# Kernel tuning notes

Measured on AMD Instinct MI355X. Metric: run time of the kernel, lower is better.

## Reference

```python
import jax, jax.numpy as jnp
import numpy as np

N = 4096      # number of stocks (token axis)
D = 512       # d_model
H = 8         # nhead
DE = 64       # d_emb
DH = D // H   # head_dim = 64
TEMP = float(np.sqrt(DH))
EPS = 1e-5


def _ln(x, g, b):
    mu = jnp.mean(x, axis=-1, keepdims=True)
    var = jnp.var(x, axis=-1, keepdims=True)
    return (x - mu) * jax.lax.rsqrt(var + EPS) * g + b


def setup_inputs() -> dict:
    key = jax.random.key(0)
    ks = jax.random.split(key, 8)
    init = lambda k, shape, fan: (jax.random.normal(k, shape, jnp.float32) / np.sqrt(fan).astype(np.float32))
    return {
        "x": jax.random.normal(ks[0], (N, D), jnp.float32),
        "industry_emb": jax.random.normal(ks[1], (N, DE), jnp.float32),
        # projection weights stored as [in, out] so y = x @ W
        "Wq": init(ks[2], (D + DE, D), D + DE),
        "Wk": init(ks[3], (D + DE, D), D + DE),
        "Wv": init(ks[4], (D, D), D),
        "g1": jnp.ones((D,), jnp.float32), "b1": jnp.zeros((D,), jnp.float32),
        "g2": jnp.ones((DE,), jnp.float32), "b2": jnp.zeros((DE,), jnp.float32),
        "g3": jnp.ones((D,), jnp.float32), "b3": jnp.zeros((D,), jnp.float32),
        "W_ffn1": init(ks[5], (D, D), D), "b_ffn1": jnp.zeros((D,), jnp.float32),
        "W_ffn2": init(ks[6], (D, D), D), "b_ffn2": jnp.zeros((D,), jnp.float32),
    }


def reference(x, industry_emb, Wq, Wk, Wv, g1, b1, g2, b2, g3, b3,
              W_ffn1, b_ffn1, W_ffn2, b_ffn2):
    xn = _ln(x, g1, b1)                       # [N, D]
    en = _ln(industry_emb, g2, b2)            # [N, DE]
    qk_in = jnp.concatenate([xn, en], axis=-1)  # [N, D+DE]
    q = (qk_in @ Wq).reshape(N, H, DH)
    k = (qk_in @ Wk).reshape(N, H, DH)
    v = (xn @ Wv).reshape(N, H, DH)
    # batched multi-head attention (equivalent to the per-head torch loop)
    scores = jnp.einsum('nhd,mhd->hnm', q, k) / TEMP   # [H, N, N]
    attn = jax.nn.softmax(scores, axis=-1)
    att = jnp.einsum('hnm,mhd->nhd', attn, v).reshape(N, D)
    xt = xn + att
    h = _ln(xt, g3, b3)
    ffn = jax.nn.relu(h @ W_ffn1 + b_ffn1) @ W_ffn2 + b_ffn2
    return xt + ffn
```

## Files before the change

kernel.cpp:

```cpp
#include <hip/hip_runtime.h>

#define NTOK 4096
#define DMODEL 512
#define DEMB 64
#define DCAT 576
#define NHEAD 8
#define DHEAD 64
#define QSCALE 0.18033688011112042f

typedef float f32x4 __attribute__((ext_vector_type(4)));
typedef float f32x16 __attribute__((ext_vector_type(16)));
typedef short s16x8 __attribute__((ext_vector_type(8)));
typedef unsigned short u16;
typedef u16 u16x4 __attribute__((ext_vector_type(4)));
typedef u16 u16x8 __attribute__((ext_vector_type(8)));
typedef unsigned int u32;

__device__ __forceinline__ u16 f2bf(float f) {
  union { float f; unsigned u; } v; v.f = f;
  unsigned r = v.u + 0x7fffu + ((v.u >> 16) & 1u);
  return (u16)(r >> 16);
}

__device__ __forceinline__ float bf2f(u16 u) {
  union { unsigned u; float f; } v; v.u = ((unsigned)u) << 16;
  return v.f;
}

__device__ __forceinline__ u32 cvtpk_bf16(float lo, float hi) {
  u32 r;
  asm("v_cvt_pk_bf16_f32 %0, %1, %2" : "=v"(r) : "v"(lo), "v"(hi));
  return r;
}

__device__ __forceinline__ void gload16(const void* g, void* lds) {
  __builtin_amdgcn_global_load_lds((const __attribute__((address_space(1))) u32*)g,
                                   (__attribute__((address_space(3))) u32*)lds, 16, 0, 0);
}

__global__ void wtrans_kernel(const float* __restrict__ Wq, const float* __restrict__ Wk,
                              const float* __restrict__ Wv, const float* __restrict__ Wf1,
                              const float* __restrict__ Wf2,
                              u16* __restrict__ Tqkv, u16* __restrict__ Tf1, u16* __restrict__ Tf2) {
  __shared__ float tile[64][65];
  int w = blockIdx.z;
  const float* src; u16* dst; int Ksrc, Kdst;
  if (w == 0)      { src = Wq;  dst = Tqkv;              Ksrc = 576; Kdst = 576; }
  else if (w == 1) { src = Wk;  dst = Tqkv + 512 * 576;  Ksrc = 576; Kdst = 576; }
  else if (w == 2) { src = Wv;  dst = Tqkv + 1024 * 576; Ksrc = 512; Kdst = 576; }
  else if (w == 3) { src = Wf1; dst = Tf1;               Ksrc = 512; Kdst = 512; }
  else             { src = Wf2; dst = Tf2;               Ksrc = 512; Kdst = 512; }
  int kb = blockIdx.x * 64;
  if (kb >= Kdst) return;
  int nb = blockIdx.y * 64;
  int tid = threadIdx.x;
  #pragma unroll
  for (int i = 0; i < 16; ++i) {
    int idx = tid + i * 256;
    int r = idx >> 6, c = idx & 63;
    tile[r][c] = (kb + r < Ksrc) ? src[(size_t)(kb + r) * DMODEL + nb + c] : 0.0f;
  }
  __syncthreads();
  #pragma unroll
  for (int i = 0; i < 16; ++i) {
    int idx = tid + i * 256;
    int r = idx >> 6, c = idx & 63;
    dst[(size_t)(nb + r) * Kdst + kb + c] = f2bf(tile[c][r]);
  }
}

__global__ void lnx_kernel(const float* __restrict__ x, const float* __restrict__ g,
                           const float* __restrict__ b, float* __restrict__ xt,
                           u16* __restrict__ qkin) {
  int row = blockIdx.x * 4 + (threadIdx.x >> 6);
  int lane = threadIdx.x & 63;
  const float* xr = x + (size_t)row * DMODEL + lane * 8;
  float v[8];
  float4 a0 = *(const float4*)xr;
  float4 a1 = *(const float4*)(xr + 4);
  v[0]=a0.x; v[1]=a0.y; v[2]=a0.z; v[3]=a0.w; v[4]=a1.x; v[5]=a1.y; v[6]=a1.z; v[7]=a1.w;
  float s = 0.f, ss = 0.f;
  #pragma unroll
  for (int j = 0; j < 8; ++j) { s += v[j]; ss += v[j]*v[j]; }
  #pragma unroll
  for (int off = 32; off > 0; off >>= 1) { s += __shfl_xor(s, off); ss += __shfl_xor(ss, off); }
  float mu = s * (1.0f / DMODEL);
  float var = ss * (1.0f / DMODEL) - mu * mu;
  float rs = rsqrtf(var + 1e-5f);
  float4 g0 = *(const float4*)(g + lane * 8);
  float4 g1v = *(const float4*)(g + lane * 8 + 4);
  float4 b0 = *(const float4*)(b + lane * 8);
  float4 b1v = *(const float4*)(b + lane * 8 + 4);
  float gg[8] = {g0.x,g0.y,g0.z,g0.w,g1v.x,g1v.y,g1v.z,g1v.w};
  float bb[8] = {b0.x,b0.y,b0.z,b0.w,b1v.x,b1v.y,b1v.z,b1v.w};
  float o[8]; u16x8 ob;
  #pragma unroll
  for (int j = 0; j < 8; ++j) { o[j] = (v[j]-mu)*rs*gg[j] + bb[j]; ob[j] = f2bf(o[j]); }
  float* xo = xt + (size_t)row * DMODEL + lane * 8;
  *(float4*)xo = make_float4(o[0],o[1],o[2],o[3]);
  *(float4*)(xo + 4) = make_float4(o[4],o[5],o[6],o[7]);
  *(u16x8*)(qkin + (size_t)row * DCAT + lane * 8) = ob;
}

__global__ void lne_kernel(const float* __restrict__ e, const float* __restrict__ g,
                           const float* __restrict__ b, u16* __restrict__ qkin) {
  int row = blockIdx.x * 4 + (threadIdx.x >> 6);
  int lane = threadIdx.x & 63;
  float v = e[(size_t)row * DEMB + lane];
  float s = v, ss = v * v;
  #pragma unroll
  for (int off = 32; off > 0; off >>= 1) { s += __shfl_xor(s, off); ss += __shfl_xor(ss, off); }
  float mu = s * (1.0f / DEMB);
  float var = ss * (1.0f / DEMB) - mu * mu;
  float rs = rsqrtf(var + 1e-5f);
  float o = (v - mu) * rs * g[lane] + b[lane];
  qkin[(size_t)row * DCAT + DMODEL + lane] = f2bf(o);
}

__global__ void ln3_kernel(float* __restrict__ xt, const float* __restrict__ g,
                           const float* __restrict__ b, u16* __restrict__ hb,
                           const u16* __restrict__ obuf, const float* __restrict__ lbuf) {
  int row = blockIdx.x * 4 + (threadIdx.x >> 6);
  int lane = threadIdx.x & 63;
  int h = lane >> 3;
  int dh0 = (lane & 7) * 8;
  float* xr = xt + (size_t)row * DMODEL + lane * 8;
  float v[8];
  float4 a0 = *(const float4*)xr;
  float4 a1 = *(const float4*)(xr + 4);
  v[0]=a0.x; v[1]=a0.y; v[2]=a0.z; v[3]=a0.w; v[4]=a1.x; v[5]=a1.y; v[6]=a1.z; v[7]=a1.w;
  float osum[8] = {};
  float lsum = 0.f;
  #pragma unroll
  for (int s = 0; s < 4; ++s) {
    size_t hb_idx = (size_t)(s * 8 + h) * NTOK + row;
    u16x8 ov = *(const u16x8*)(obuf + hb_idx * 64 + dh0);
    lsum += lbuf[hb_idx];
    #pragma unroll
    for (int j = 0; j < 8; ++j) osum[j] += bf2f(ov[j]);
  }
  float rcpl = 1.0f / lsum;
  #pragma unroll
  for (int j = 0; j < 8; ++j) v[j] += osum[j] * rcpl;
  *(float4*)xr = make_float4(v[0],v[1],v[2],v[3]);
  *(float4*)(xr + 4) = make_float4(v[4],v[5],v[6],v[7]);
  float s = 0.f, ss = 0.f;
  #pragma unroll
  for (int j = 0; j < 8; ++j) { s += v[j]; ss += v[j]*v[j]; }
  #pragma unroll
  for (int off = 32; off > 0; off >>= 1) { s += __shfl_xor(s, off); ss += __shfl_xor(ss, off); }
  float mu = s * (1.0f / DMODEL);
  float var = ss * (1.0f / DMODEL) - mu * mu;
  float rs = rsqrtf(var + 1e-5f);
  float4 g0 = *(const float4*)(g + lane * 8);
  float4 g1v = *(const float4*)(g + lane * 8 + 4);
  float4 b0 = *(const float4*)(b + lane * 8);
  float4 b1v = *(const float4*)(b + lane * 8 + 4);
  float gg[8] = {g0.x,g0.y,g0.z,g0.w,g1v.x,g1v.y,g1v.z,g1v.w};
  float bb[8] = {b0.x,b0.y,b0.z,b0.w,b1v.x,b1v.y,b1v.z,b1v.w};
  u16x8 ob;
  #pragma unroll
  for (int j = 0; j < 8; ++j) ob[j] = f2bf((v[j]-mu)*rs*gg[j] + bb[j]);
  *(u16x8*)(hb + (size_t)row * DMODEL + lane * 8) = ob;
}

__global__ __launch_bounds__(256) void gemm_qkv_kernel(
    const u16* __restrict__ A, const u16* __restrict__ Bt, u16* __restrict__ outb) {
  __shared__ __align__(16) u16 smem[12288];
  u16* Al = smem;
  u16* Bl = smem + 8192;
  int tid = threadIdx.x, lane = tid & 63, wid = tid >> 6;
  int li = lane & 15, g4 = lane >> 4;
  int n0 = blockIdx.x * 64, m0 = blockIdx.y * 128;
  int wr = (wid >> 1) * 64, wc = (wid & 1) * 32;
  f32x4 acc[4][2] = {};
  for (int k0 = 0; k0 < DCAT; k0 += 64) {
    #pragma unroll
    for (int i = 0; i < 4; ++i) {
      int idx = i * 256 + tid;
      int row = idx >> 3, cb = (idx & 7) * 8;
      gload16(A + (size_t)(m0 + row) * DCAT + k0 + cb, (char*)Al + idx * 16);
    }
    #pragma unroll
    for (int i = 0; i < 2; ++i) {
      int idx = i * 256 + tid;
      int row = idx >> 3, cb = (idx & 7) * 8;
      gload16(Bt + (size_t)(n0 + row) * DCAT + k0 + cb, (char*)Bl + idx * 16);
    }
    __syncthreads();
    #pragma unroll
    for (int kk = 0; kk < 2; ++kk) {
      s16x8 af[4], bfv[2];
      #pragma unroll
      for (int mi = 0; mi < 4; ++mi)
        af[mi] = *(const s16x8*)&Al[(wr + mi * 16 + li) * 64 + kk * 32 + g4 * 8];
      #pragma unroll
      for (int ni = 0; ni < 2; ++ni)
        bfv[ni] = *(const s16x8*)&Bl[(wc + ni * 16 + li) * 64 + kk * 32 + g4 * 8];
      #pragma unroll
      for (int mi = 0; mi < 4; ++mi)
        #pragma unroll
        for (int ni = 0; ni < 2; ++ni)
          acc[mi][ni] = __builtin_amdgcn_mfma_f32_16x16x32_bf16(af[mi], bfv[ni], acc[mi][ni], 0, 0, 0);
    }
    __syncthreads();
  }
  if (n0 < 1024) {
    float scale = (n0 < 512) ? QSCALE : 1.0f;
    int nb = (n0 < 512) ? n0 : n0 - 512;
    u16* dst = outb + ((n0 < 512) ? 0 : (size_t)NTOK * DMODEL);
    #pragma unroll
    for (int mi = 0; mi < 4; ++mi)
      #pragma unroll
      for (int ni = 0; ni < 2; ++ni) {
        int col = nb + wc + ni * 16 + li;
        int h = col >> 6, dh = col & 63;
        #pragma unroll
        for (int r = 0; r < 4; ++r) {
          int row = m0 + wr + mi * 16 + g4 * 4 + r;
          dst[((size_t)h * NTOK + row) * DHEAD + dh] = f2bf(acc[mi][ni][r] * scale);
        }
      }
  } else {
    u16* vT = outb + (size_t)2 * NTOK * DMODEL;
    u16* tp = smem;
    __syncthreads();
    #pragma unroll
    for (int mi = 0; mi < 4; ++mi)
      #pragma unroll
      for (int ni = 0; ni < 2; ++ni) {
        int cl = wc + ni * 16 + li;
        int r0 = wr + mi * 16 + g4 * 4;
        int r0p = (r0 & ~12) | ((r0 & 4) << 1) | ((r0 & 8) >> 1);
        u16x4 pk;
        pk[0] = f2bf(acc[mi][ni][0]); pk[1] = f2bf(acc[mi][ni][1]);
        pk[2] = f2bf(acc[mi][ni][2]); pk[3] = f2bf(acc[mi][ni][3]);
        *(u16x4*)&tp[cl * 136 + r0p] = pk;
      }
    __syncthreads();
    for (int c = tid; c < 1024; c += 256) {
      int cl = c >> 4, seg = c & 15;
      u16x8 v = *(const u16x8*)&tp[cl * 136 + seg * 8];
      *(u16x8*)&vT[(size_t)(n0 - 1024 + cl) * NTOK + m0 + seg * 8] = v;
    }
  }
}

template<int MODE>
__global__ __launch_bounds__(256) void gemm_kernel(
    const u16* __restrict__ A, int lda, const u16* __restrict__ Bt, int K,
    u16* __restrict__ outb, float* __restrict__ outf,
    const float* __restrict__ bias, const float* __restrict__ xt) {
  __shared__ __align__(16) u16 smem[8192];
  u16* Al = smem;
  u16* Bl = smem + 4096;
  int tid = threadIdx.x, lane = tid & 63, wid = tid >> 6;
  int li = lane & 15, g4 = lane >> 4;
  int n0 = blockIdx.x * 64, m0 = blockIdx.y * 64;
  int wr = (wid >> 1) * 32, wc = (wid & 1) * 32;
  f32x4 acc[2][2] = {};
  for (int k0 = 0; k0 < K; k0 += 64) {
    #pragma unroll
    for (int i = 0; i < 2; ++i) {
      int idx = i * 256 + tid;
      int row = idx >> 3, cb = (idx & 7) * 8;
      gload16(A + (size_t)(m0 + row) * lda + k0 + cb, (char*)Al + idx * 16);
    }
    #pragma unroll
    for (int i = 0; i < 2; ++i) {
      int idx = i * 256 + tid;
      int row = idx >> 3, cb = (idx & 7) * 8;
      gload16(Bt + (size_t)(n0 + row) * K + k0 + cb, (char*)Bl + idx * 16);
    }
    __syncthreads();
    #pragma unroll
    for (int kk = 0; kk < 2; ++kk) {
      s16x8 af[2], bfv[2];
      #pragma unroll
      for (int mi = 0; mi < 2; ++mi)
        af[mi] = *(const s16x8*)&Al[(wr + mi * 16 + li) * 64 + kk * 32 + g4 * 8];
      #pragma unroll
      for (int ni = 0; ni < 2; ++ni)
        bfv[ni] = *(const s16x8*)&Bl[(wc + ni * 16 + li) * 64 + kk * 32 + g4 * 8];
      #pragma unroll
      for (int mi = 0; mi < 2; ++mi)
        #pragma unroll
        for (int ni = 0; ni < 2; ++ni)
          acc[mi][ni] = __builtin_amdgcn_mfma_f32_16x16x32_bf16(af[mi], bfv[ni], acc[mi][ni], 0, 0, 0);
    }
    __syncthreads();
  }
  #pragma unroll
  for (int mi = 0; mi < 2; ++mi)
    #pragma unroll
    for (int ni = 0; ni < 2; ++ni) {
      int col = n0 + wc + ni * 16 + li;
      float bv = bias[col];
      #pragma unroll
      for (int r = 0; r < 4; ++r) {
        int row = m0 + wr + mi * 16 + g4 * 4 + r;
        float v = acc[mi][ni][r] + bv;
        if (MODE == 3) {
          v = fmaxf(v, 0.0f);
          outb[(size_t)row * DMODEL + col] = f2bf(v);
        } else {
          outf[(size_t)row * DMODEL + col] = v + xt[(size_t)row * DMODEL + col];
        }
      }
    }
}

__global__ __launch_bounds__(512, 1) void attn_kernel(
    const u16* __restrict__ qh, const u16* __restrict__ kh,
    const u16* __restrict__ vT, u16* __restrict__ obuf, float* __restrict__ lbuf) {
  __shared__ __align__(16) u16 kbufT[2][4096];
  __shared__ __align__(16) u16 vbufT[2][4096];
  int tid = threadIdx.x, lane = tid & 63, w = tid >> 6;
  int lq = lane & 31, h5 = lane >> 5;
  int h = blockIdx.x & 7, ks = (blockIdx.x >> 3) & 3, qt = blockIdx.x >> 5;
  int q0w = qt * 256 + w * 32;
  int ko0 = ks * 1024;
  const u16* qb = qh + ((size_t)h * NTOK + q0w + lq) * DHEAD;
  s16x8 qf[4];
  #pragma unroll
  for (int kc = 0; kc < 4; ++kc)
    qf[kc] = *(const s16x8*)(qb + kc * 16 + h5 * 8);
  f32x16 o[2] = {};
  float lsum = 0.f;
  const char* kh_b = (const char*)(kh + (size_t)h * NTOK * DHEAD);
  const char* v_b = (const char*)(vT + (size_t)h * DHEAD * NTOK);

  auto stage = [&](int c, int ko) {
    int lo6 = tid & 63, r6 = tid >> 6;
    gload16(kh_b + (size_t)(ko + lo6) * 128 + r6 * 16, (char*)&kbufT[c][0] + tid * 16);
    gload16(v_b + (size_t)lo6 * (NTOK * 2) + (size_t)(ko + r6 * 8) * 2,
            (char*)&vbufT[c][0] + tid * 16);
  };

  stage(0, ko0);
  asm volatile("s_waitcnt vmcnt(0)" ::: "memory");
  __builtin_amdgcn_sched_barrier(0);
  __syncthreads();

  for (int t = 0; t < 16; ++t) {
    int cur = t & 1;
    if (t < 15) stage(cur ^ 1, ko0 + (t + 1) * 64);
    const u16* Kl = &kbufT[cur][0];
    const u16* Vl = &vbufT[cur][0];
    #pragma unroll
    for (int kb2 = 0; kb2 < 2; ++kb2) {
      f32x16 st = {};
      #pragma unroll
      for (int kc = 0; kc < 4; ++kc) {
        s16x8 kf = *(const s16x8*)(Kl + ((kc * 2 + h5) * 64 + kb2 * 32 + lq) * 8);
        st = __builtin_amdgcn_mfma_f32_32x32x16_bf16(kf, qf[kc], st, 0, 0, 0);
      }
      float p[16];
      #pragma unroll
      for (int r = 0; r < 16; ++r) { p[r] = __builtin_amdgcn_exp2f(st[r]); lsum += p[r]; }
      #pragma unroll
      for (int cl = 0; cl < 2; ++cl) {
        int b = cl * 8;
        union { u32 wv[4]; s16x8 hv; } pu;
        pu.wv[0] = cvtpk_bf16(p[b + 0], p[b + 1]);
        pu.wv[1] = cvtpk_bf16(p[b + 2], p[b + 3]);
        pu.wv[2] = cvtpk_bf16(p[b + 4], p[b + 5]);
        pu.wv[3] = cvtpk_bf16(p[b + 6], p[b + 7]);
        int kcg = kb2 * 2 + cl;
        #pragma unroll
        for (int dhalf = 0; dhalf < 2; ++dhalf) {
          s16x8 bv = *(const s16x8*)(Vl + ((kcg * 2 + h5) * 64 + dhalf * 32 + lq) * 8);
          o[dhalf] = __builtin_amdgcn_mfma_f32_32x32x16_bf16(pu.hv, bv, o[dhalf], 0, 0, 0);
        }
      }
    }
    if (t < 15) {
      asm volatile("s_waitcnt vmcnt(0)" ::: "memory");
      __builtin_amdgcn_sched_barrier(0);
      __syncthreads();
    }
  }

  lsum += __shfl_xor(lsum, 32);
  size_t slice = (size_t)(ks * 8 + h) * NTOK;
  if (h5 == 0) lbuf[slice + q0w + lq] = lsum;
  u16* ob = obuf + (slice + q0w) * 64;
  #pragma unroll
  for (int dhalf = 0; dhalf < 2; ++dhalf)
    #pragma unroll
    for (int r = 0; r < 16; ++r) {
      int crow = (r & 3) + 8 * (r >> 2) + 4 * h5;
      ob[(size_t)crow * 64 + dhalf * 32 + lq] = f2bf(o[dhalf][r]);
    }
}

extern "C" void kernel_launch(void* const* d_in, const int* in_sizes, int n_in,
                              void* d_out, int out_size, void* d_ws, size_t ws_size,
                              hipStream_t stream) {
  const float* x   = (const float*)d_in[0];
  const float* emb = (const float*)d_in[1];
  const float* Wq  = (const float*)d_in[2];
  const float* Wk  = (const float*)d_in[3];
  const float* Wv  = (const float*)d_in[4];
  const float* g1  = (const float*)d_in[5];
  const float* b1  = (const float*)d_in[6];
  const float* g2  = (const float*)d_in[7];
  const float* b2  = (const float*)d_in[8];
  const float* g3  = (const float*)d_in[9];
  const float* b3  = (const float*)d_in[10];
  const float* Wf1 = (const float*)d_in[11];
  const float* bf1 = (const float*)d_in[12];
  const float* Wf2 = (const float*)d_in[13];
  const float* bf2 = (const float*)d_in[14];
  float* out = (float*)d_out;

  char* ws = (char*)d_ws;
  size_t off = 0;
  auto alloc = [&](size_t bytes) { void* p = ws + off; off += (bytes + 255) & ~255ull; return p; };
  float* xt = (float*)alloc((size_t)NTOK * DMODEL * 4);
  u16* qkin = (u16*)alloc((size_t)NTOK * DCAT * 2);
  u16* hb   = (u16*)alloc((size_t)NTOK * DMODEL * 2);
  u16* r1   = (u16*)alloc((size_t)NTOK * DMODEL * 2);
  u16* qkvh = (u16*)alloc((size_t)3 * NTOK * DMODEL * 2);
  u16* Tqkv = (u16*)alloc((size_t)1536 * DCAT * 2);
  u16* Tf1  = (u16*)alloc((size_t)DMODEL * DMODEL * 2);
  u16* Tf2  = (u16*)alloc((size_t)DMODEL * DMODEL * 2);
  u16* obuf = (u16*)alloc((size_t)4 * NHEAD * NTOK * DHEAD * 2);
  float* lbuf = (float*)alloc((size_t)4 * NHEAD * NTOK * 4);
  u16* qhd = qkvh;
  u16* khd = qkvh + (size_t)NTOK * DMODEL;
  u16* vTd = qkvh + (size_t)2 * NTOK * DMODEL;

  wtrans_kernel<<<dim3(9, 8, 5), 256, 0, stream>>>(Wq, Wk, Wv, Wf1, Wf2, Tqkv, Tf1, Tf2);
  lnx_kernel<<<1024, 256, 0, stream>>>(x, g1, b1, xt, qkin);
  lne_kernel<<<1024, 256, 0, stream>>>(emb, g2, b2, qkin);
  gemm_qkv_kernel<<<dim3(24, 32), 256, 0, stream>>>(qkin, Tqkv, qkvh);
  attn_kernel<<<512, 512, 0, stream>>>(qhd, khd, vTd, obuf, lbuf);
  ln3_kernel<<<1024, 256, 0, stream>>>(xt, g3, b3, hb, obuf, lbuf);
  gemm_kernel<3><<<dim3(8, 64), 256, 0, stream>>>(hb, DMODEL, Tf1, DMODEL, r1, nullptr, bf1, nullptr);
  gemm_kernel<4><<<dim3(8, 64), 256, 0, stream>>>(r1, DMODEL, Tf2, DMODEL, nullptr, out, bf2, xt);
}
```

Before: 102.2 us.

## Fuse prep kernels and process two query tiles per attention wave

Merges the weight transpose and both input layernorm kernels into one launch using block-index ranges, removing two kernel launches. The attention kernel now uses 4 waves of 256 threads, each handling 64 query rows as two 32-row groups. Each K and V fragment read from LDS is reused across both groups, cutting LDS traffic per MFMA. The cost is twice the accumulator and Q-fragment registers per wave, and fewer waves per block to hide latency.

```diff
diff --git a/kernel.cpp b/kernel.cpp
--- a/kernel.cpp
+++ b/kernel.cpp
@@ -38,83 +38,85 @@
                                    (__attribute__((address_space(3))) u32*)lds, 16, 0, 0);
 }
 
-__global__ void wtrans_kernel(const float* __restrict__ Wq, const float* __restrict__ Wk,
-                              const float* __restrict__ Wv, const float* __restrict__ Wf1,
-                              const float* __restrict__ Wf2,
-                              u16* __restrict__ Tqkv, u16* __restrict__ Tf1, u16* __restrict__ Tf2) {
+__global__ void prep_kernel(const float* __restrict__ x, const float* __restrict__ emb,
+                            const float* __restrict__ Wq, const float* __restrict__ Wk,
+                            const float* __restrict__ Wv, const float* __restrict__ Wf1,
+                            const float* __restrict__ Wf2,
+                            const float* __restrict__ g1, const float* __restrict__ b1,
+                            const float* __restrict__ g2, const float* __restrict__ b2,
+                            float* __restrict__ xt, u16* __restrict__ qkin,
+                            u16* __restrict__ Tqkv, u16* __restrict__ Tf1,
+                            u16* __restrict__ Tf2) {
   __shared__ float tile[64][65];
-  int w = blockIdx.z;
-  const float* src; u16* dst; int Ksrc, Kdst;
-  if (w == 0)      { src = Wq;  dst = Tqkv;              Ksrc = 576; Kdst = 576; }
-  else if (w == 1) { src = Wk;  dst = Tqkv + 512 * 576;  Ksrc = 576; Kdst = 576; }
-  else if (w == 2) { src = Wv;  dst = Tqkv + 1024 * 576; Ksrc = 512; Kdst = 576; }
-  else if (w == 3) { src = Wf1; dst = Tf1;               Ksrc = 512; Kdst = 512; }
-  else             { src = Wf2; dst = Tf2;               Ksrc = 512; Kdst = 512; }
-  int kb = blockIdx.x * 64;
-  if (kb >= Kdst) return;
-  int nb = blockIdx.y * 64;
+  int b = blockIdx.x;
   int tid = threadIdx.x;
-  #pragma unroll
-  for (int i = 0; i < 16; ++i) {
-    int idx = tid + i * 256;
-    int r = idx >> 6, c = idx & 63;
-    tile[r][c] = (kb + r < Ksrc) ? src[(size_t)(kb + r) * DMODEL + nb + c] : 0.0f;
-  }
-  __syncthreads();
-  #pragma unroll
-  for (int i = 0; i < 16; ++i) {
-    int idx = tid + i * 256;
-    int r = idx >> 6, c = idx & 63;
-    dst[(size_t)(nb + r) * Kdst + kb + c] = f2bf(tile[c][r]);
-  }
-}
-
-__global__ void lnx_kernel(const float* __restrict__ x, const float* __restrict__ g,
-                           const float* __restrict__ b, float* __restrict__ xt,
-                           u16* __restrict__ qkin) {
-  int row = blockIdx.x * 4 + (threadIdx.x >> 6);
-  int lane = threadIdx.x & 63;
-  const float* xr = x + (size_t)row * DMODEL + lane * 8;
-  float v[8];
-  float4 a0 = *(const float4*)xr;
-  float4 a1 = *(const float4*)(xr + 4);
-  v[0]=a0.x; v[1]=a0.y; v[2]=a0.z; v[3]=a0.w; v[4]=a1.x; v[5]=a1.y; v[6]=a1.z; v[7]=a1.w;
-  float s = 0.f, ss = 0.f;
-  #pragma unroll
-  for (int j = 0; j < 8; ++j) { s += v[j]; ss += v[j]*v[j]; }
-  #pragma unroll
-  for (int off = 32; off > 0; off >>= 1) { s += __shfl_xor(s, off); ss += __shfl_xor(ss, off); }
-  float mu = s * (1.0f / DMODEL);
-  float var = ss * (1.0f / DMODEL) - mu * mu;
-  float rs = rsqrtf(var + 1e-5f);
-  float4 g0 = *(const float4*)(g + lane * 8);
-  float4 g1v = *(const float4*)(g + lane * 8 + 4);
-  float4 b0 = *(const float4*)(b + lane * 8);
-  float4 b1v = *(const float4*)(b + lane * 8 + 4);
-  float gg[8] = {g0.x,g0.y,g0.z,g0.w,g1v.x,g1v.y,g1v.z,g1v.w};
-  float bb[8] = {b0.x,b0.y,b0.z,b0.w,b1v.x,b1v.y,b1v.z,b1v.w};
-  float o[8]; u16x8 ob;
-  #pragma unroll
-  for (int j = 0; j < 8; ++j) { o[j] = (v[j]-mu)*rs*gg[j] + bb[j]; ob[j] = f2bf(o[j]); }
-  float* xo = xt + (size_t)row * DMODEL + lane * 8;
-  *(float4*)xo = make_float4(o[0],o[1],o[2],o[3]);
-  *(float4*)(xo + 4) = make_float4(o[4],o[5],o[6],o[7]);
-  *(u16x8*)(qkin + (size_t)row * DCAT + lane * 8) = ob;
-}
-
-__global__ void lne_kernel(const float* __restrict__ e, const float* __restrict__ g,
-                           const float* __restrict__ b, u16* __restrict__ qkin) {
-  int row = blockIdx.x * 4 + (threadIdx.x >> 6);
-  int lane = threadIdx.x & 63;
-  float v = e[(size_t)row * DEMB + lane];
-  float s = v, ss = v * v;
-  #pragma unroll
-  for (int off = 32; off > 0; off >>= 1) { s += __shfl_xor(s, off); ss += __shfl_xor(ss, off); }
-  float mu = s * (1.0f / DEMB);
-  float var = ss * (1.0f / DEMB) - mu * mu;
-  float rs = rsqrtf(var + 1e-5f);
-  float o = (v - mu) * rs * g[lane] + b[lane];
-  qkin[(size_t)row * DCAT + DMODEL + lane] = f2bf(o);
+  if (b < 360) {
+    int w = b / 72, r = b % 72;
+    int kbi = r % 9, nbi = r / 9;
+    const float* src; u16* dst; int Ksrc, Kdst;
+    if (w == 0)      { src = Wq;  dst = Tqkv;              Ksrc = 576; Kdst = 576; }
+    else if (w == 1) { src = Wk;  dst = Tqkv + 512 * 576;  Ksrc = 576; Kdst = 576; }
+    else if (w == 2) { src = Wv;  dst = Tqkv + 1024 * 576; Ksrc = 512; Kdst = 576; }
+    else if (w == 3) { src = Wf1; dst = Tf1;               Ksrc = 512; Kdst = 512; }
+    else             { src = Wf2; dst = Tf2;               Ksrc = 512; Kdst = 512; }
+    int kb = kbi * 64;
+    if (kb >= Kdst) return;
+    int nb = nbi * 64;
+    #pragma unroll
+    for (int i = 0; i < 16; ++i) {
+      int idx = tid + i * 256;
+      int rr = idx >> 6, c = idx & 63;
+      tile[rr][c] = (kb + rr < Ksrc) ? src[(size_t)(kb + rr) * DMODEL + nb + c] : 0.0f;
+    }
+    __syncthreads();
+    #pragma unroll
+    for (int i = 0; i < 16; ++i) {
+      int idx = tid + i * 256;
+      int rr = idx >> 6, c = idx & 63;
+      dst[(size_t)(nb + rr) * Kdst + kb + c] = f2bf(tile[c][rr]);
+    }
+  } else if (b < 1384) {
+    int row = (b - 360) * 4 + (tid >> 6);
+    int lane = tid & 63;
+    const float* xr = x + (size_t)row * DMODEL + lane * 8;
+    float v[8];
+    float4 a0 = *(const float4*)xr;
+    float4 a1 = *(const float4*)(xr + 4);
+    v[0]=a0.x; v[1]=a0.y; v[2]=a0.z; v[3]=a0.w; v[4]=a1.x; v[5]=a1.y; v[6]=a1.z; v[7]=a1.w;
+    float s = 0.f, ss = 0.f;
+    #pragma unroll
+    for (int j = 0; j < 8; ++j) { s += v[j]; ss += v[j]*v[j]; }
+    #pragma unroll
+    for (int off = 32; off > 0; off >>= 1) { s += __shfl_xor(s, off); ss += __shfl_xor(ss, off); }
+    float mu = s * (1.0f / DMODEL);
+    float var = ss * (1.0f / DMODEL) - mu * mu;
+    float rs = rsqrtf(var + 1e-5f);
+    float4 g0 = *(const float4*)(g1 + lane * 8);
+    float4 g1v = *(const float4*)(g1 + lane * 8 + 4);
+    float4 b0 = *(const float4*)(b1 + lane * 8);
+    float4 b1v = *(const float4*)(b1 + lane * 8 + 4);
+    float gg[8] = {g0.x,g0.y,g0.z,g0.w,g1v.x,g1v.y,g1v.z,g1v.w};
+    float bb[8] = {b0.x,b0.y,b0.z,b0.w,b1v.x,b1v.y,b1v.z,b1v.w};
+    float o[8]; u16x8 ob;
+    #pragma unroll
+    for (int j = 0; j < 8; ++j) { o[j] = (v[j]-mu)*rs*gg[j] + bb[j]; ob[j] = f2bf(o[j]); }
+    float* xo = xt + (size_t)row * DMODEL + lane * 8;
+    *(float4*)xo = make_float4(o[0],o[1],o[2],o[3]);
+    *(float4*)(xo + 4) = make_float4(o[4],o[5],o[6],o[7]);
+    *(u16x8*)(qkin + (size_t)row * DCAT + lane * 8) = ob;
+  } else {
+    int row = (b - 1384) * 4 + (tid >> 6);
+    int lane = tid & 63;
+    float v = emb[(size_t)row * DEMB + lane];
+    float s = v, ss = v * v;
+    #pragma unroll
+    for (int off = 32; off > 0; off >>= 1) { s += __shfl_xor(s, off); ss += __shfl_xor(ss, off); }
+    float mu = s * (1.0f / DEMB);
+    float var = ss * (1.0f / DEMB) - mu * mu;
+    float rs = rsqrtf(var + 1e-5f);
+    float o = (v - mu) * rs * g2[lane] + b2[lane];
+    qkin[(size_t)row * DCAT + DMODEL + lane] = f2bf(o);
+  }
 }
 
 __global__ void ln3_kernel(float* __restrict__ xt, const float* __restrict__ g,
@@ -310,7 +312,7 @@
     }
 }
 
-__global__ __launch_bounds__(512, 1) void attn_kernel(
+__global__ __launch_bounds__(256, 1) void attn_kernel(
     const u16* __restrict__ qh, const u16* __restrict__ kh,
     const u16* __restrict__ vT, u16* __restrict__ obuf, float* __restrict__ lbuf) {
   __shared__ __align__(16) u16 kbufT[2][4096];
@@ -318,23 +320,30 @@
   int tid = threadIdx.x, lane = tid & 63, w = tid >> 6;
   int lq = lane & 31, h5 = lane >> 5;
   int h = blockIdx.x & 7, ks = (blockIdx.x >> 3) & 3, qt = blockIdx.x >> 5;
-  int q0w = qt * 256 + w * 32;
+  int q0w = qt * 256 + w * 64;
   int ko0 = ks * 1024;
-  const u16* qb = qh + ((size_t)h * NTOK + q0w + lq) * DHEAD;
-  s16x8 qf[4];
-  #pragma unroll
-  for (int kc = 0; kc < 4; ++kc)
-    qf[kc] = *(const s16x8*)(qb + kc * 16 + h5 * 8);
-  f32x16 o[2] = {};
-  float lsum = 0.f;
+  s16x8 qf[2][4];
+  #pragma unroll
+  for (int g = 0; g < 2; ++g) {
+    const u16* qb = qh + ((size_t)h * NTOK + q0w + g * 32 + lq) * DHEAD;
+    #pragma unroll
+    for (int kc = 0; kc < 4; ++kc)
+      qf[g][kc] = *(const s16x8*)(qb + kc * 16 + h5 * 8);
+  }
+  f32x16 o[2][2] = {};
+  float lsum[2] = {0.f, 0.f};
   const char* kh_b = (const char*)(kh + (size_t)h * NTOK * DHEAD);
   const char* v_b = (const char*)(vT + (size_t)h * DHEAD * NTOK);
 
   auto stage = [&](int c, int ko) {
-    int lo6 = tid & 63, r6 = tid >> 6;
-    gload16(kh_b + (size_t)(ko + lo6) * 128 + r6 * 16, (char*)&kbufT[c][0] + tid * 16);
-    gload16(v_b + (size_t)lo6 * (NTOK * 2) + (size_t)(ko + r6 * 8) * 2,
-            (char*)&vbufT[c][0] + tid * 16);
+    #pragma unroll
+    for (int i = 0; i < 2; ++i) {
+      int s = tid + i * 256;
+      int lo6 = s & 63, r6 = s >> 6;
+      gload16(kh_b + (size_t)(ko + lo6) * 128 + r6 * 16, (char*)&kbufT[c][0] + s * 16);
+      gload16(v_b + (size_t)lo6 * (NTOK * 2) + (size_t)(ko + r6 * 8) * 2,
+              (char*)&vbufT[c][0] + s * 16);
+    }
   };
 
   stage(0, ko0);
@@ -349,28 +358,44 @@
     const u16* Vl = &vbufT[cur][0];
     #pragma unroll
     for (int kb2 = 0; kb2 < 2; ++kb2) {
-      f32x16 st = {};
-      #pragma unroll
-      for (int kc = 0; kc < 4; ++kc) {
-        s16x8 kf = *(const s16x8*)(Kl + ((kc * 2 + h5) * 64 + kb2 * 32 + lq) * 8);
-        st = __builtin_amdgcn_mfma_f32_32x32x16_bf16(kf, qf[kc], st, 0, 0, 0);
-      }
-      float p[16];
-      #pragma unroll
-      for (int r = 0; r < 16; ++r) { p[r] = __builtin_amdgcn_exp2f(st[r]); lsum += p[r]; }
+      s16x8 kf[4];
+      #pragma unroll
+      for (int kc = 0; kc < 4; ++kc)
+        kf[kc] = *(const s16x8*)(Kl + ((kc * 2 + h5) * 64 + kb2 * 32 + lq) * 8);
+      u32 pw[2][2][4];
+      #pragma unroll
+      for (int g = 0; g < 2; ++g) {
+        f32x16 st = {};
+        #pragma unroll
+        for (int kc = 0; kc < 4; ++kc)
+          st = __builtin_amdgcn_mfma_f32_32x32x16_bf16(kf[kc], qf[g][kc], st, 0, 0, 0);
+        float p[16];
+        float rs = 0.f;
+        #pragma unroll
+        for (int r = 0; r < 16; ++r) { p[r] = __builtin_amdgcn_exp2f(st[r]); rs += p[r]; }
+        lsum[g] += rs;
+        #pragma unroll
+        for (int cl = 0; cl < 2; ++cl) {
+          int bb = cl * 8;
+          pw[g][cl][0] = cvtpk_bf16(p[bb + 0], p[bb + 1]);
+          pw[g][cl][1] = cvtpk_bf16(p[bb + 2], p[bb + 3]);
+          pw[g][cl][2] = cvtpk_bf16(p[bb + 4], p[bb + 5]);
+          pw[g][cl][3] = cvtpk_bf16(p[bb + 6], p[bb + 7]);
+        }
+      }
       #pragma unroll
       for (int cl = 0; cl < 2; ++cl) {
-        int b = cl * 8;
-        union { u32 wv[4]; s16x8 hv; } pu;
-        pu.wv[0] = cvtpk_bf16(p[b + 0], p[b + 1]);
-        pu.wv[1] = cvtpk_bf16(p[b + 2], p[b + 3]);
-        pu.wv[2] = cvtpk_bf16(p[b + 4], p[b + 5]);
-        pu.wv[3] = cvtpk_bf16(p[b + 6], p[b + 7]);
         int kcg = kb2 * 2 + cl;
         #pragma unroll
         for (int dhalf = 0; dhalf < 2; ++dhalf) {
           s16x8 bv = *(const s16x8*)(Vl + ((kcg * 2 + h5) * 64 + dhalf * 32 + lq) * 8);
-          o[dhalf] = __builtin_amdgcn_mfma_f32_32x32x16_bf16(pu.hv, bv, o[dhalf], 0, 0, 0);
+          #pragma unroll
+          for (int g = 0; g < 2; ++g) {
+            union { u32 wv[4]; s16x8 hv; } pu;
+            pu.wv[0] = pw[g][cl][0]; pu.wv[1] = pw[g][cl][1];
+            pu.wv[2] = pw[g][cl][2]; pu.wv[3] = pw[g][cl][3];
+            o[g][dhalf] = __builtin_amdgcn_mfma_f32_32x32x16_bf16(pu.hv, bv, o[g][dhalf], 0, 0, 0);
+          }
         }
       }
     }
@@ -381,17 +406,20 @@
     }
   }
 
-  lsum += __shfl_xor(lsum, 32);
   size_t slice = (size_t)(ks * 8 + h) * NTOK;
-  if (h5 == 0) lbuf[slice + q0w + lq] = lsum;
-  u16* ob = obuf + (slice + q0w) * 64;
-  #pragma unroll
-  for (int dhalf = 0; dhalf < 2; ++dhalf)
-    #pragma unroll
-    for (int r = 0; r < 16; ++r) {
-      int crow = (r & 3) + 8 * (r >> 2) + 4 * h5;
-      ob[(size_t)crow * 64 + dhalf * 32 + lq] = f2bf(o[dhalf][r]);
-    }
+  #pragma unroll
+  for (int g = 0; g < 2; ++g) {
+    float v = lsum[g] + __shfl_xor(lsum[g], 32);
+    if (h5 == 0) lbuf[slice + q0w + g * 32 + lq] = v;
+    u16* ob = obuf + (slice + q0w + g * 32) * 64;
+    #pragma unroll
+    for (int dhalf = 0; dhalf < 2; ++dhalf)
+      #pragma unroll
+      for (int r = 0; r < 16; ++r) {
+        int crow = (r & 3) + 8 * (r >> 2) + 4 * h5;
+        ob[(size_t)crow * 64 + dhalf * 32 + lq] = f2bf(o[g][dhalf][r]);
+      }
+  }
 }
 
 extern "C" void kernel_launch(void* const* d_in, const int* in_sizes, int n_in,
@@ -431,11 +459,10 @@
   u16* khd = qkvh + (size_t)NTOK * DMODEL;
   u16* vTd = qkvh + (size_t)2 * NTOK * DMODEL;
 
-  wtrans_kernel<<<dim3(9, 8, 5), 256, 0, stream>>>(Wq, Wk, Wv, Wf1, Wf2, Tqkv, Tf1, Tf2);
-  lnx_kernel<<<1024, 256, 0, stream>>>(x, g1, b1, xt, qkin);
-  lne_kernel<<<1024, 256, 0, stream>>>(emb, g2, b2, qkin);
+  prep_kernel<<<2408, 256, 0, stream>>>(x, emb, Wq, Wk, Wv, Wf1, Wf2,
+                                        g1, b1, g2, b2, xt, qkin, Tqkv, Tf1, Tf2);
   gemm_qkv_kernel<<<dim3(24, 32), 256, 0, stream>>>(qkin, Tqkv, qkvh);
-  attn_kernel<<<512, 512, 0, stream>>>(qhd, khd, vTd, obuf, lbuf);
+  attn_kernel<<<512, 256, 0, stream>>>(qhd, khd, vTd, obuf, lbuf);
   ln3_kernel<<<1024, 256, 0, stream>>>(xt, g3, b3, hb, obuf, lbuf);
   gemm_kernel<3><<<dim3(8, 64), 256, 0, stream>>>(hb, DMODEL, Tf1, DMODEL, r1, nullptr, bf1, nullptr);
   gemm_kernel<4><<<dim3(8, 64), 256, 0, stream>>>(r1, DMODEL, Tf2, DMODEL, nullptr, out, bf2, xt);
```

Result: slower. 118.2 us (+15.7%).
